# Kernel optimization log

Measured on AMD Instinct MI355X. Metric: run time of the kernel, lower is better.

## Reference

```python
import jax, jax.numpy as jnp
import numpy as np

E = 16      # num_experts
K = 4       # num_experts_per_tok
H = 2048    # hidden_size
I = 1408    # moe_intermediate_size
SI = 5632   # shared expert intermediate size
CAP = 1024
NORM_TOPK = False


def setup_inputs() -> dict:
    key = jax.random.key(0)
    ks = jax.random.split(key, 9)
    def w(k, shape, fan_in):
        return jax.random.normal(k, shape, jnp.float32) * (fan_in ** -0.5)
    return {
        "hidden_states": jax.random.normal(ks[0], (1, 2048, H), jnp.float32),
        "gate_w":  w(ks[1], (E, H), H),        # router: Linear(H -> E), no bias
        "we_gate": w(ks[2], (E, I, H), H),     # per-expert gate_proj weights
        "we_up":   w(ks[3], (E, I, H), H),     # per-expert up_proj weights
        "we_down": w(ks[4], (E, H, I), I),     # per-expert down_proj weights
        "ws_gate": w(ks[5], (SI, H), H),       # shared expert gate_proj
        "ws_up":   w(ks[6], (SI, H), H),       # shared expert up_proj
        "ws_down": w(ks[7], (H, SI), SI),      # shared expert down_proj
        "sg_w":    w(ks[8], (1, H), H),        # shared_expert_gate: Linear(H -> 1)
    }


def reference(hidden_states, gate_w, we_gate, we_up, we_down,
              ws_gate, ws_up, ws_down, sg_w):
    B, S, Hd = hidden_states.shape
    x = hidden_states.reshape(-1, Hd)                      # [T, H]
    T = x.shape[0]

    # --- router ---
    router_logits = x @ gate_w.T                           # [T, E]
    probs = jax.nn.softmax(router_logits.astype(jnp.float32), axis=-1)
    topw, topi = jax.lax.top_k(probs, K)                   # [T, K]
    if NORM_TOPK:
        topw = topw / topw.sum(axis=-1, keepdims=True)

    # --- dispatch: flatten (token, slot) assignments ---
    A = T * K
    fe = topi.reshape(A)                                   # expert id per assignment
    fw = topw.reshape(A)                                   # routing weight per assignment
    ft = jnp.repeat(jnp.arange(T), K)                      # token id per assignment
    # position of each assignment within its expert (rank in arrival order)
    oh = jax.nn.one_hot(fe, E, dtype=jnp.int32)            # [A, E]
    pos = jnp.take_along_axis(jnp.cumsum(oh, axis=0) - 1, fe[:, None], axis=1)[:, 0]
    valid = pos < CAP
    # scatter tokens into per-expert buffers; overflow goes to dummy row CAP
    buf = jnp.zeros((E, CAP + 1, Hd), x.dtype)
    buf = buf.at[fe, jnp.where(valid, pos, CAP)].set(x[ft])[:, :CAP]  # [E, C, H]

    # --- per-expert SiLU-gated MLP (batched grouped GEMMs) ---
    g = jnp.einsum('ech,eih->eci', buf, we_gate)
    u = jnp.einsum('ech,eih->eci', buf, we_up)
    eo = jnp.einsum('eci,ehi->ech', jax.nn.silu(g) * u, we_down)      # [E, C, H]

    # --- combine: weighted scatter-add back to tokens ---
    ga = eo[fe, jnp.minimum(pos, CAP - 1)]                 # [A, H]
    wcomb = (fw * valid.astype(fw.dtype)).astype(x.dtype)
    y = jnp.zeros((T, Hd), x.dtype).at[ft].add(ga * wcomb[:, None])

    # --- shared expert with sigmoid gate ---
    sh = (jax.nn.silu(x @ ws_gate.T) * (x @ ws_up.T)) @ ws_down.T
    sh = jax.nn.sigmoid(x @ sg_w.T) * sh

    out = (y + sh).reshape(B, S, Hd)
    return out, router_logits
```

## Files before the change

### kernel.cpp

```cpp
#include <hip/hip_runtime.h>

#define T_TOK 2048
#define NE 16
#define KTOP 4
#define HD 2048
#define ID 1408
#define SID 5632
#define CAPACITY 1024

typedef __attribute__((ext_vector_type(8))) short short8;
typedef __attribute__((ext_vector_type(4))) float floatx4;

__device__ __forceinline__ short f2b(float f){
  union { float f; unsigned u; } v; v.f = f;
  unsigned r = v.u + 0x7fffu + ((v.u >> 16) & 1u);
  return (short)(r >> 16);
}
__device__ __forceinline__ float b2f(short s){
  union { float f; unsigned u; } v; v.u = ((unsigned)(unsigned short)s) << 16;
  return v.f;
}
__device__ __forceinline__ unsigned cvt_pk(float a, float b){
  unsigned r;
  asm("v_cvt_pk_bf16_f32 %0, %1, %2" : "=v"(r) : "v"(a), "v"(b));
  return r;
}
__device__ __forceinline__ short8 cvt8(float4 a, float4 b){
  union { unsigned d[4]; short8 s; } u;
  u.d[0] = cvt_pk(a.x, a.y); u.d[1] = cvt_pk(a.z, a.w);
  u.d[2] = cvt_pk(b.x, b.y); u.d[3] = cvt_pk(b.z, b.w);
  return u.s;
}
__device__ __forceinline__ void gl16(const void* g, void* l){
  __builtin_amdgcn_global_load_lds(
      (const __attribute__((address_space(1))) void*)g,
      (__attribute__((address_space(3))) void*)l, 16, 0, 0);
}

__device__ __forceinline__ void conv_range(
    int cb, int ncb,
    const float* __restrict__ s1, short* __restrict__ d1, long long n1,
    const float* __restrict__ s2, short* __restrict__ d2, long long n2)
{
  const long long tot = n1 + n2;
  const long long stride = (long long)ncb * 256;
  #pragma unroll 2
  for (long long i = (long long)cb * 256 + threadIdx.x; i < tot; i += stride){
    const float* s; short8* d; long long j;
    if (i < n1){ s = s1; d = (short8*)d1; j = i; }
    else       { s = s2; d = (short8*)d2; j = i - n1; }
    float4 f0 = ((const float4*)s)[j * 2];
    float4 f1 = ((const float4*)s)[j * 2 + 1];
    d[j] = cvt8(f0, f1);
  }
}

__global__ void moe_zero(int* __restrict__ counts){
  if (threadIdx.x < NE) counts[threadIdx.x] = 0;
}

__global__ void moe_router(const float* __restrict__ x,
                           const float* __restrict__ gate_w,
                           const float* __restrict__ sg_w,
                           float* __restrict__ logits_out,
                           short* __restrict__ xb,
                           int* __restrict__ counts,
                           int* __restrict__ slot_token,
                           int* __restrict__ tslot,
                           float* __restrict__ tw,
                           float* __restrict__ sg,
                           const float* cs1, short* cd1, long long cn1,
                           const float* cs2, short* cd2, long long cn2)
{
  if (blockIdx.x >= 512){
    conv_range(blockIdx.x - 512, gridDim.x - 512, cs1, cd1, cn1, cs2, cd2, cn2);
    return;
  }
  int wave = threadIdx.x >> 6, lane = threadIdx.x & 63;
  int t = (blockIdx.x << 2) + wave;
  const float4* xr = (const float4*)(x + (size_t)t * HD);
  short8* xbw = (short8*)(xb + (size_t)t * HD);
  float acc[17];
  #pragma unroll
  for (int e = 0; e < 17; ++e) acc[e] = 0.f;
  #pragma unroll
  for (int j = 0; j < 4; ++j){
    int i4 = (j * 64 + lane) * 2;
    float4 x0 = xr[i4], x1 = xr[i4 + 1];
    xbw[j * 64 + lane] = cvt8(x0, x1);
    #pragma unroll
    for (int e = 0; e < 16; ++e){
      const float4* gr = (const float4*)(gate_w + e * HD);
      float4 g0 = gr[i4], g1 = gr[i4 + 1];
      acc[e] += x0.x*g0.x + x0.y*g0.y + x0.z*g0.z + x0.w*g0.w
              + x1.x*g1.x + x1.y*g1.y + x1.z*g1.z + x1.w*g1.w;
    }
    const float4* sr = (const float4*)sg_w;
    float4 s0 = sr[i4], s1 = sr[i4 + 1];
    acc[16] += x0.x*s0.x + x0.y*s0.y + x0.z*s0.z + x0.w*s0.w
             + x1.x*s1.x + x1.y*s1.y + x1.z*s1.z + x1.w*s1.w;
  }
  #pragma unroll
  for (int e = 0; e < 17; ++e){
    float v = acc[e];
    #pragma unroll
    for (int off = 32; off > 0; off >>= 1) v += __shfl_xor(v, off, 64);
    acc[e] = v;
  }
  if (lane == 0){
    float m = acc[0];
    #pragma unroll
    for (int e = 1; e < 16; ++e) m = fmaxf(m, acc[e]);
    float p[16]; float s = 0.f;
    #pragma unroll
    for (int e = 0; e < 16; ++e){ p[e] = expf(acc[e] - m); s += p[e]; }
    float inv = 1.f / s;
    #pragma unroll
    for (int e = 0; e < 16; ++e) logits_out[t * 16 + e] = acc[e];
    unsigned used = 0;
    for (int k = 0; k < KTOP; ++k){
      float best = -1.f; int bi = 0;
      #pragma unroll
      for (int e = 0; e < 16; ++e){
        float pe = ((used >> e) & 1u) ? -1.f : p[e];
        if (pe > best){ best = pe; bi = e; }
      }
      used |= (1u << bi);
      int pos = atomicAdd(&counts[bi], 1);
      int enc = -1;
      if (pos < CAPACITY){
        slot_token[bi * CAPACITY + pos] = t;
        enc = bi * CAPACITY + pos;
      }
      tslot[t * KTOP + k] = enc;
      tw[t * KTOP + k] = best * inv;
    }
    sg[t] = 1.f / (1.f + expf(-acc[16]));
  }
}


#define GEMM_PREAMBLE \
  const int tid = threadIdx.x; \
  const int lane = tid & 63, wave = tid >> 6; \
  const int wr = wave >> 1, wc = wave & 1; \
  const int lrow = lane & 15, lk = lane >> 4; \
  const int s_th = (tid & 7) ^ ((tid >> 3) & 7); \
  const int koff = (s_th & 3) << 3; \
  const int rloc = ((tid >> 3) << 1) + (s_th >> 2); \
  const int lb = lrow >> 1; \
  const int soff = (((((lrow & 1) << 2) | lk) ^ (lb & 7)) << 4); \
  const int abase = (wr * 32 + lb) * 128 + soff;

#define WAIT8  asm volatile("s_waitcnt vmcnt(8)" ::: "memory");
#define WAIT6  asm volatile("s_waitcnt vmcnt(6)" ::: "memory");
#define WAIT4  asm volatile("s_waitcnt vmcnt(4)" ::: "memory");
#define WAIT3  asm volatile("s_waitcnt vmcnt(3)" ::: "memory");
#define WAIT0  asm volatile("s_waitcnt vmcnt(0)" ::: "memory");
#define SBAR   asm volatile("s_barrier" ::: "memory");

__global__ __launch_bounds__(256) void moe_gateup(
    const short* __restrict__ Asrc,
    const short* __restrict__ Wg, const short* __restrict__ Wu,
    short* __restrict__ Out,
    const int* __restrict__ counts, const int* __restrict__ slot_token,
    int Ndim, int Kdim, int expert_mode, int mtiles, int ntiles,
    const float* cs1, short* cd1, long long cn1,
    const float* cs2, short* cd2, long long cn2, int conv_nwg)
{
  if ((int)blockIdx.x < conv_nwg){
    conv_range(blockIdx.x, conv_nwg, cs1, cd1, cn1, cs2, cd2, cn2);
    return;
  }
  int nwg = gridDim.x - conv_nwg;
  int bid = blockIdx.x - conv_nwg;
  int wg = ((bid & 7) * (nwg >> 3)) + (bid >> 3);
  int m_t = wg % mtiles; wg /= mtiles;
  int n_t = wg % ntiles; int e = wg / ntiles;

  int cnt = T_TOK; size_t woff = 0; short* out = Out;
  if (expert_mode){
    cnt = counts[e]; if (cnt > CAPACITY) cnt = CAPACITY;
    if (m_t * 128 >= cnt) return;
    woff = (size_t)e * Ndim * Kdim;
    out = Out + (size_t)e * CAPACITY * Ndim;
  }
  const int m0 = m_t * 128, n0 = n_t * 64;

  __shared__ __align__(16) char smem[3][16384];

  GEMM_PREAMBLE
  const int gbase = 8192 + (wc * 16 + lb) * 128 + soff;

  const short* aP0;
  const short* aP1;
  {
    int p0 = m0 + rloc, p1 = m0 + 64 + rloc;
    if (expert_mode){
      int q0 = (p0 < cnt) ? p0 : 0, q1 = (p1 < cnt) ? p1 : 0;
      aP0 = Asrc + (size_t)slot_token[e * CAPACITY + q0] * Kdim + koff;
      aP1 = Asrc + (size_t)slot_token[e * CAPACITY + q1] * Kdim + koff;
    } else {
      aP0 = Asrc + (size_t)p0 * Kdim + koff;
      aP1 = Asrc + (size_t)p1 * Kdim + koff;
    }
  }
  const short* bgP = Wg + woff + (size_t)(n0 + rloc) * Kdim + koff;
  const short* buP = Wu + woff + (size_t)(n0 + rloc) * Kdim + koff;

  const floatx4 vzero = {0.f, 0.f, 0.f, 0.f};
  floatx4 accg[4][2], accu[4][2];
  #pragma unroll
  for (int i = 0; i < 4; ++i)
    #pragma unroll
    for (int j = 0; j < 2; ++j){ accg[i][j] = vzero; accu[i][j] = vzero; }

#define GU_ISSUE(B, T) { char* _b = (B); const int _k = (T) << 5; \
    gl16(aP0 + _k, _b + tid * 16); \
    gl16(aP1 + _k, _b + 4096 + tid * 16); \
    gl16(bgP + _k, _b + 8192 + tid * 16); \
    gl16(buP + _k, _b + 12288 + tid * 16); }

#define GU_COMPUTE(B) { const char* bb = (B); \
    short8 a[4], bg[2], bu[2]; \
    _Pragma("unroll") \
    for (int mf = 0; mf < 4; ++mf) a[mf] = *(const short8*)(bb + abase + mf * 1024); \
    _Pragma("unroll") \
    for (int nf = 0; nf < 2; ++nf){ \
      bg[nf] = *(const short8*)(bb + gbase + nf * 1024); \
      bu[nf] = *(const short8*)(bb + gbase + 4096 + nf * 1024); } \
    _Pragma("unroll") \
    for (int mf = 0; mf < 4; ++mf) \
      _Pragma("unroll") \
      for (int nf = 0; nf < 2; ++nf){ \
        accg[mf][nf] = __builtin_amdgcn_mfma_f32_16x16x32_bf16(a[mf], bg[nf], accg[mf][nf], 0, 0, 0); \
        accu[mf][nf] = __builtin_amdgcn_mfma_f32_16x16x32_bf16(a[mf], bu[nf], accu[mf][nf], 0, 0, 0); } }

  const int NSTEP = Kdim >> 5;
  char* b0 = smem[0];
  char* b1 = smem[1];
  char* b2 = smem[2];
  GU_ISSUE(b0, 0)
  GU_ISSUE(b1, 1)
  for (int s = 0; s < NSTEP; ++s){
    if (s + 2 < NSTEP){ GU_ISSUE(b2, s + 2) WAIT8 }
    else if (s + 2 == NSTEP){ WAIT4 }
    else { WAIT0 }
    SBAR
    GU_COMPUTE(b0)
    SBAR
    char* t = b0; b0 = b1; b1 = b2; b2 = t;
  }

  const int colbase = n0 + wc * 32 + lrow;
  #pragma unroll
  for (int mf = 0; mf < 4; ++mf){
    int pr = m0 + wr * 64 + mf * 16 + lk * 4;
    #pragma unroll
    for (int nf = 0; nf < 2; ++nf){
      floatx4 g4 = accg[mf][nf], u4 = accu[mf][nf];
      int col = colbase + nf * 16;
      #pragma unroll
      for (int r = 0; r < 4; ++r){
        float gv = g4[r], uv = u4[r];
        float a = (gv / (1.f + __expf(-gv))) * uv;
        out[(size_t)(pr + r) * Ndim + col] = f2b(a);
      }
    }
  }
}

template<int NF>
__global__ __launch_bounds__(256) void moe_down(
    const short* __restrict__ Asrc, const short* __restrict__ Wd,
    float* __restrict__ y, short* __restrict__ eo,
    const int* __restrict__ counts, const int* __restrict__ slot_token,
    const float* __restrict__ sgate,
    int Kdim, int expert_mode, int mtiles, int ntiles)
{
  int nwg = gridDim.x;
  int wg = ((blockIdx.x & 7) * (nwg >> 3)) + (blockIdx.x >> 3);
  int m_t = wg % mtiles; wg /= mtiles;
  int n_t = wg % ntiles; int e = wg / ntiles;

  int cnt = T_TOK; const short* ab = Asrc; size_t woff = 0;
  if (expert_mode){
    cnt = counts[e]; if (cnt > CAPACITY) cnt = CAPACITY;
    if (m_t * 128 >= cnt) return;
    ab = Asrc + (size_t)e * CAPACITY * Kdim;
    woff = (size_t)e * HD * Kdim;
  }
  const int m0 = m_t * 128, n0 = n_t * (NF * 32);

  __shared__ __align__(16) char smem[3][8192 + NF * 2048];

  GEMM_PREAMBLE
  const int bbase = 8192 + (wc * (NF * 8) + lb) * 128 + soff;

  const short* aP0 = ab + (size_t)(m0 + rloc) * Kdim + koff;
  const short* aP1 = ab + (size_t)(m0 + 64 + rloc) * Kdim + koff;
  const short* bP0 = Wd + woff + (size_t)(n0 + rloc) * Kdim + koff;
  const short* bP1 = (NF == 4) ? (Wd + woff + (size_t)(n0 + 64 + rloc) * Kdim + koff) : bP0;

  const floatx4 vzero = {0.f, 0.f, 0.f, 0.f};
  floatx4 acc[4][NF];
  #pragma unroll
  for (int i = 0; i < 4; ++i)
    #pragma unroll
    for (int j = 0; j < NF; ++j) acc[i][j] = vzero;

#define DN_ISSUE(B, T) { char* _b = (B); const int _k = (T) << 5; \
    gl16(aP0 + _k, _b + tid * 16); \
    gl16(aP1 + _k, _b + 4096 + tid * 16); \
    gl16(bP0 + _k, _b + 8192 + tid * 16); \
    if (NF == 4) gl16(bP1 + _k, _b + 12288 + tid * 16); }

#define DN_COMPUTE(B) { const char* bb = (B); \
    short8 a[4], b[NF]; \
    _Pragma("unroll") \
    for (int mf = 0; mf < 4; ++mf) a[mf] = *(const short8*)(bb + abase + mf * 1024); \
    _Pragma("unroll") \
    for (int nf = 0; nf < NF; ++nf) b[nf] = *(const short8*)(bb + bbase + nf * 1024); \
    _Pragma("unroll") \
    for (int mf = 0; mf < 4; ++mf) \
      _Pragma("unroll") \
      for (int nf = 0; nf < NF; ++nf) \
        acc[mf][nf] = __builtin_amdgcn_mfma_f32_16x16x32_bf16(a[mf], b[nf], acc[mf][nf], 0, 0, 0); }

  const int NSTEP = Kdim >> 5;
  char* b0 = smem[0];
  char* b1 = smem[1];
  char* b2 = smem[2];
  DN_ISSUE(b0, 0)
  DN_ISSUE(b1, 1)
  for (int s = 0; s < NSTEP; ++s){
    if (s + 2 < NSTEP){
      DN_ISSUE(b2, s + 2)
      if (NF == 4){ WAIT8 } else { WAIT6 }
    } else if (s + 2 == NSTEP){
      if (NF == 4){ WAIT4 } else { WAIT3 }
    } else { WAIT0 }
    SBAR
    DN_COMPUTE(b0)
    SBAR
    char* t = b0; b0 = b1; b1 = b2; b2 = t;
  }

  const int colb = n0 + wc * (NF * 16) + lrow;
  if (expert_mode){
    #pragma unroll
    for (int mf = 0; mf < 4; ++mf){
      int pr = m0 + wr * 64 + mf * 16 + lk * 4;
      #pragma unroll
      for (int r = 0; r < 4; ++r){
        int p = pr + r;
        #pragma unroll
        for (int nf = 0; nf < NF; ++nf)
          eo[(size_t)(e * CAPACITY + p) * HD + colb + nf * 16] = f2b(acc[mf][nf][r]);
      }
    }
  } else {
    #pragma unroll
    for (int mf = 0; mf < 4; ++mf){
      int pr = m0 + wr * 64 + mf * 16 + lk * 4;
      #pragma unroll
      for (int r = 0; r < 4; ++r){
        int t = pr + r;
        float sv = sgate[t];
        #pragma unroll
        for (int nf = 0; nf < NF; ++nf)
          y[(size_t)t * HD + colb + nf * 16] = sv * acc[mf][nf][r];
      }
    }
  }
}

__global__ void moe_combine(const short* __restrict__ eo,
                            const int* __restrict__ tslot,
                            const float* __restrict__ tw,
                            float* __restrict__ y)
{
  int t = blockIdx.x;
  int o = threadIdx.x << 3;
  float* yp = y + (size_t)t * HD + o;
  float4 a0 = *(const float4*)yp, a1 = *(const float4*)(yp + 4);
  float acc[8] = {a0.x, a0.y, a0.z, a0.w, a1.x, a1.y, a1.z, a1.w};
  #pragma unroll
  for (int k = 0; k < KTOP; ++k){
    int s = tslot[t * KTOP + k];
    if (s >= 0){
      float w = tw[t * KTOP + k];
      short8 v = *(const short8*)(eo + (size_t)s * HD + o);
      #pragma unroll
      for (int j = 0; j < 8; ++j) acc[j] += w * b2f(v[j]);
    }
  }
  float4 r0 = {acc[0], acc[1], acc[2], acc[3]};
  float4 r1 = {acc[4], acc[5], acc[6], acc[7]};
  *(float4*)yp = r0; *(float4*)(yp + 4) = r1;
}

extern "C" void kernel_launch(void* const* d_in, const int* in_sizes, int n_in,
                              void* d_out, int out_size, void* d_ws, size_t ws_size,
                              hipStream_t stream)
{
  (void)in_sizes; (void)n_in; (void)out_size; (void)ws_size;
  const float* x       = (const float*)d_in[0];
  const float* gate_w  = (const float*)d_in[1];
  const float* we_gate = (const float*)d_in[2];
  const float* we_up   = (const float*)d_in[3];
  const float* we_down = (const float*)d_in[4];
  const float* wsg     = (const float*)d_in[5];
  const float* wsu     = (const float*)d_in[6];
  const float* wsd     = (const float*)d_in[7];
  const float* sg_w    = (const float*)d_in[8];

  float* y      = (float*)d_out;
  float* logits = y + (size_t)T_TOK * HD;

  const size_t N_EW = (size_t)NE * ID * HD;
  const size_t N_SW = (size_t)SID * HD;
  const long long G_EW = (long long)(N_EW / 8);
  const long long G_SW = (long long)(N_SW / 8);

  char* ws = (char*)d_ws;
  size_t off = 0;
  short* xb   = (short*)(ws + off); off += (size_t)T_TOK * HD * 2;
  short* wb   = (short*)(ws + off); off += (3 * N_EW + 3 * N_SW) * 2;
  short* act  = (short*)(ws + off); off += (size_t)NE * CAPACITY * ID * 2;
  short* acts = (short*)(ws + off); off += (size_t)T_TOK * SID * 2;
  int*   slot_token = (int*)  (ws + off); off += 65536;
  int*   tslot      = (int*)  (ws + off); off += 32768;
  float* tw         = (float*)(ws + off); off += 32768;
  int*   counts     = (int*)  (ws + off); off += 256;
  float* sg         = (float*)(ws + off);

  short* wbeg = wb;
  short* wbeu = wb + N_EW;
  short* wbed = wb + 2 * N_EW;
  short* wbsg = wb + 3 * N_EW;
  short* wbsu = wb + 3 * N_EW + N_SW;
  short* wbsd = wb + 3 * N_EW + 2 * N_SW;
  short* eo = wbeg;

  moe_zero<<<1, 64, 0, stream>>>(counts);
  moe_router<<<512 + 512, 256, 0, stream>>>(x, gate_w, sg_w, logits, xb,
                                            counts, slot_token, tslot, tw, sg,
                                            wsg, wbsg, G_SW, wsu, wbsu, G_SW);
  moe_gateup<<<512 + 16 * 88, 256, 0, stream>>>(xb, wbsg, wbsu, acts,
                                                nullptr, nullptr, SID, HD, 0, 16, 88,
                                                we_gate, wbeg, G_EW, we_up, wbeu, G_EW, 512);
  moe_gateup<<<512 + 8 * 22 * NE, 256, 0, stream>>>(xb, wbeg, wbeu, act,
                                                    counts, slot_token, ID, HD, 1, 8, 22,
                                                    we_down, wbed, G_EW, wsd, wbsd, G_SW, 512);
  moe_down<2><<<16 * 32, 256, 0, stream>>>(acts, wbsd, y, nullptr, nullptr, nullptr,
                                           sg, SID, 0, 16, 32);
  moe_down<4><<<8 * 16 * NE, 256, 0, stream>>>(act, wbed, y, eo, counts, slot_token,
                                               nullptr, ID, 1, 8, 16);
  moe_combine<<<T_TOK, 256, 0, stream>>>(eo, tslot, tw, y);
}
```

Before: 759.6 us.

## Load fp32 weights directly into GEMMs and convert to bf16 in-register

Removes the separate fp32-to-bf16 weight conversion passes that were folded into the router and gate/up launches. The GEMM kernels now stream fp32 weight tiles into LDS and convert them to bf16 while building MFMA operands. This drops the full write and re-read of bf16 weight copies, at the cost of twice the weight bytes per tile in the GEMM loops. The LDS pipeline also goes from triple to double buffering to fit the larger fp32 tiles, which reduces load/compute overlap.

After: 918.4 us. +20.9%, slower.

```diff
diff --git a/kernel.cpp b/kernel.cpp
--- a/kernel.cpp
+++ b/kernel.cpp
@@ -35,24 +35,6 @@
   __builtin_amdgcn_global_load_lds(
       (const __attribute__((address_space(1))) void*)g,
       (__attribute__((address_space(3))) void*)l, 16, 0, 0);
-}
-
-__device__ __forceinline__ void conv_range(
-    int cb, int ncb,
-    const float* __restrict__ s1, short* __restrict__ d1, long long n1,
-    const float* __restrict__ s2, short* __restrict__ d2, long long n2)
-{
-  const long long tot = n1 + n2;
-  const long long stride = (long long)ncb * 256;
-  #pragma unroll 2
-  for (long long i = (long long)cb * 256 + threadIdx.x; i < tot; i += stride){
-    const float* s; short8* d; long long j;
-    if (i < n1){ s = s1; d = (short8*)d1; j = i; }
-    else       { s = s2; d = (short8*)d2; j = i - n1; }
-    float4 f0 = ((const float4*)s)[j * 2];
-    float4 f1 = ((const float4*)s)[j * 2 + 1];
-    d[j] = cvt8(f0, f1);
-  }
 }
 
 __global__ void moe_zero(int* __restrict__ counts){
@@ -68,14 +50,8 @@
                            int* __restrict__ slot_token,
                            int* __restrict__ tslot,
                            float* __restrict__ tw,
-                           float* __restrict__ sg,
-                           const float* cs1, short* cd1, long long cn1,
-                           const float* cs2, short* cd2, long long cn2)
+                           float* __restrict__ sg)
 {
-  if (blockIdx.x >= 512){
-    conv_range(blockIdx.x - 512, gridDim.x - 512, cs1, cd1, cn1, cs2, cd2, cn2);
-    return;
-  }
   int wave = threadIdx.x >> 6, lane = threadIdx.x & 63;
   int t = (blockIdx.x << 2) + wave;
   const float4* xr = (const float4*)(x + (size_t)t * HD);
@@ -150,31 +126,26 @@
   const int rloc = ((tid >> 3) << 1) + (s_th >> 2); \
   const int lb = lrow >> 1; \
   const int soff = (((((lrow & 1) << 2) | lk) ^ (lb & 7)) << 4); \
-  const int abase = (wr * 32 + lb) * 128 + soff;
-
-#define WAIT8  asm volatile("s_waitcnt vmcnt(8)" ::: "memory");
+  const int abase = (wr * 32 + lb) * 128 + soff; \
+  const int srow8 = tid >> 3; \
+  const int bls = (tid & 7) ^ (srow8 & 7); \
+  const int xr_ = lrow & 7; \
+  const int sl0 = ((lk << 1) ^ xr_) << 4, sl1 = (((lk << 1) | 1) ^ xr_) << 4;
+
 #define WAIT6  asm volatile("s_waitcnt vmcnt(6)" ::: "memory");
 #define WAIT4  asm volatile("s_waitcnt vmcnt(4)" ::: "memory");
-#define WAIT3  asm volatile("s_waitcnt vmcnt(3)" ::: "memory");
 #define WAIT0  asm volatile("s_waitcnt vmcnt(0)" ::: "memory");
 #define SBAR   asm volatile("s_barrier" ::: "memory");
 
 __global__ __launch_bounds__(256) void moe_gateup(
     const short* __restrict__ Asrc,
-    const short* __restrict__ Wg, const short* __restrict__ Wu,
+    const float* __restrict__ Wg, const float* __restrict__ Wu,
     short* __restrict__ Out,
     const int* __restrict__ counts, const int* __restrict__ slot_token,
-    int Ndim, int Kdim, int expert_mode, int mtiles, int ntiles,
-    const float* cs1, short* cd1, long long cn1,
-    const float* cs2, short* cd2, long long cn2, int conv_nwg)
+    int Ndim, int Kdim, int expert_mode, int mtiles, int ntiles)
 {
-  if ((int)blockIdx.x < conv_nwg){
-    conv_range(blockIdx.x, conv_nwg, cs1, cd1, cn1, cs2, cd2, cn2);
-    return;
-  }
-  int nwg = gridDim.x - conv_nwg;
-  int bid = blockIdx.x - conv_nwg;
-  int wg = ((bid & 7) * (nwg >> 3)) + (bid >> 3);
+  int nwg = gridDim.x;
+  int wg = ((blockIdx.x & 7) * (nwg >> 3)) + (blockIdx.x >> 3);
   int m_t = wg % mtiles; wg /= mtiles;
   int n_t = wg % ntiles; int e = wg / ntiles;
 
@@ -187,10 +158,9 @@
   }
   const int m0 = m_t * 128, n0 = n_t * 64;
 
-  __shared__ __align__(16) char smem[3][16384];
+  __shared__ __align__(16) char smem[2][24576];
 
   GEMM_PREAMBLE
-  const int gbase = 8192 + (wc * 16 + lb) * 128 + soff;
 
   const short* aP0;
   const short* aP1;
@@ -205,8 +175,14 @@
       aP1 = Asrc + (size_t)p1 * Kdim + koff;
     }
   }
-  const short* bgP = Wg + woff + (size_t)(n0 + rloc) * Kdim + koff;
-  const short* buP = Wu + woff + (size_t)(n0 + rloc) * Kdim + koff;
+  const float* bgP0 = Wg + woff + (size_t)(n0 + srow8) * Kdim + bls * 4;
+  const float* bgP1 = Wg + woff + (size_t)(n0 + 32 + srow8) * Kdim + bls * 4;
+  const float* buP0 = Wu + woff + (size_t)(n0 + srow8) * Kdim + bls * 4;
+  const float* buP1 = Wu + woff + (size_t)(n0 + 32 + srow8) * Kdim + bls * 4;
+
+  const int rg0 = wc * 32 + lrow, rg1 = rg0 + 16;
+  const int o00 = rg0 * 128 + sl0, o01 = rg0 * 128 + sl1;
+  const int o10 = rg1 * 128 + sl0, o11 = rg1 * 128 + sl1;
 
   const floatx4 vzero = {0.f, 0.f, 0.f, 0.f};
   floatx4 accg[4][2], accu[4][2];
@@ -218,17 +194,19 @@
 #define GU_ISSUE(B, T) { char* _b = (B); const int _k = (T) << 5; \
     gl16(aP0 + _k, _b + tid * 16); \
     gl16(aP1 + _k, _b + 4096 + tid * 16); \
-    gl16(bgP + _k, _b + 8192 + tid * 16); \
-    gl16(buP + _k, _b + 12288 + tid * 16); }
+    gl16(bgP0 + _k, _b + 8192 + tid * 16); \
+    gl16(bgP1 + _k, _b + 12288 + tid * 16); \
+    gl16(buP0 + _k, _b + 16384 + tid * 16); \
+    gl16(buP1 + _k, _b + 20480 + tid * 16); }
 
 #define GU_COMPUTE(B) { const char* bb = (B); \
     short8 a[4], bg[2], bu[2]; \
     _Pragma("unroll") \
     for (int mf = 0; mf < 4; ++mf) a[mf] = *(const short8*)(bb + abase + mf * 1024); \
-    _Pragma("unroll") \
-    for (int nf = 0; nf < 2; ++nf){ \
-      bg[nf] = *(const short8*)(bb + gbase + nf * 1024); \
-      bu[nf] = *(const short8*)(bb + gbase + 4096 + nf * 1024); } \
+    bg[0] = cvt8(*(const float4*)(bb + 8192 + o00), *(const float4*)(bb + 8192 + o01)); \
+    bg[1] = cvt8(*(const float4*)(bb + 8192 + o10), *(const float4*)(bb + 8192 + o11)); \
+    bu[0] = cvt8(*(const float4*)(bb + 16384 + o00), *(const float4*)(bb + 16384 + o01)); \
+    bu[1] = cvt8(*(const float4*)(bb + 16384 + o10), *(const float4*)(bb + 16384 + o11)); \
     _Pragma("unroll") \
     for (int mf = 0; mf < 4; ++mf) \
       _Pragma("unroll") \
@@ -237,19 +215,13 @@
         accu[mf][nf] = __builtin_amdgcn_mfma_f32_16x16x32_bf16(a[mf], bu[nf], accu[mf][nf], 0, 0, 0); } }
 
   const int NSTEP = Kdim >> 5;
-  char* b0 = smem[0];
-  char* b1 = smem[1];
-  char* b2 = smem[2];
-  GU_ISSUE(b0, 0)
-  GU_ISSUE(b1, 1)
+  GU_ISSUE(smem[0], 0)
   for (int s = 0; s < NSTEP; ++s){
-    if (s + 2 < NSTEP){ GU_ISSUE(b2, s + 2) WAIT8 }
-    else if (s + 2 == NSTEP){ WAIT4 }
+    if (s + 1 < NSTEP){ GU_ISSUE(smem[(s + 1) & 1], s + 1) WAIT6 }
     else { WAIT0 }
     SBAR
-    GU_COMPUTE(b0)
+    GU_COMPUTE(smem[s & 1])
     SBAR
-    char* t = b0; b0 = b1; b1 = b2; b2 = t;
   }
 
   const int colbase = n0 + wc * 32 + lrow;
@@ -272,7 +244,7 @@
 
 template<int NF>
 __global__ __launch_bounds__(256) void moe_down(
-    const short* __restrict__ Asrc, const short* __restrict__ Wd,
+    const short* __restrict__ Asrc, const float* __restrict__ Wd,
     float* __restrict__ y, short* __restrict__ eo,
     const int* __restrict__ counts, const int* __restrict__ slot_token,
     const float* __restrict__ sgate,
@@ -292,15 +264,23 @@
   }
   const int m0 = m_t * 128, n0 = n_t * (NF * 32);
 
-  __shared__ __align__(16) char smem[3][8192 + NF * 2048];
+  __shared__ __align__(16) char smem[2][8192 + NF * 4096];
 
   GEMM_PREAMBLE
-  const int bbase = 8192 + (wc * (NF * 8) + lb) * 128 + soff;
 
   const short* aP0 = ab + (size_t)(m0 + rloc) * Kdim + koff;
   const short* aP1 = ab + (size_t)(m0 + 64 + rloc) * Kdim + koff;
-  const short* bP0 = Wd + woff + (size_t)(n0 + rloc) * Kdim + koff;
-  const short* bP1 = (NF == 4) ? (Wd + woff + (size_t)(n0 + 64 + rloc) * Kdim + koff) : bP0;
+  const float* bP[NF];
+  #pragma unroll
+  for (int i = 0; i < NF; ++i)
+    bP[i] = Wd + woff + (size_t)(n0 + i * 32 + srow8) * Kdim + bls * 4;
+
+  int bo0[NF], bo1[NF];
+  #pragma unroll
+  for (int nf = 0; nf < NF; ++nf){
+    int r = wc * (NF * 16) + nf * 16 + lrow;
+    bo0[nf] = r * 128 + sl0; bo1[nf] = r * 128 + sl1;
+  }
 
   const floatx4 vzero = {0.f, 0.f, 0.f, 0.f};
   floatx4 acc[4][NF];
@@ -312,15 +292,18 @@
 #define DN_ISSUE(B, T) { char* _b = (B); const int _k = (T) << 5; \
     gl16(aP0 + _k, _b + tid * 16); \
     gl16(aP1 + _k, _b + 4096 + tid * 16); \
-    gl16(bP0 + _k, _b + 8192 + tid * 16); \
-    if (NF == 4) gl16(bP1 + _k, _b + 12288 + tid * 16); }
+    _Pragma("unroll") \
+    for (int i = 0; i < NF; ++i) \
+      gl16(bP[i] + _k, _b + 8192 + i * 4096 + tid * 16); }
 
 #define DN_COMPUTE(B) { const char* bb = (B); \
     short8 a[4], b[NF]; \
     _Pragma("unroll") \
     for (int mf = 0; mf < 4; ++mf) a[mf] = *(const short8*)(bb + abase + mf * 1024); \
     _Pragma("unroll") \
-    for (int nf = 0; nf < NF; ++nf) b[nf] = *(const short8*)(bb + bbase + nf * 1024); \
+    for (int nf = 0; nf < NF; ++nf) \
+      b[nf] = cvt8(*(const float4*)(bb + 8192 + bo0[nf]), \
+                   *(const float4*)(bb + 8192 + bo1[nf])); \
     _Pragma("unroll") \
     for (int mf = 0; mf < 4; ++mf) \
       _Pragma("unroll") \
@@ -328,22 +311,15 @@
         acc[mf][nf] = __builtin_amdgcn_mfma_f32_16x16x32_bf16(a[mf], b[nf], acc[mf][nf], 0, 0, 0); }
 
   const int NSTEP = Kdim >> 5;
-  char* b0 = smem[0];
-  char* b1 = smem[1];
-  char* b2 = smem[2];
-  DN_ISSUE(b0, 0)
-  DN_ISSUE(b1, 1)
+  DN_ISSUE(smem[0], 0)
   for (int s = 0; s < NSTEP; ++s){
-    if (s + 2 < NSTEP){
-      DN_ISSUE(b2, s + 2)
-      if (NF == 4){ WAIT8 } else { WAIT6 }
-    } else if (s + 2 == NSTEP){
-      if (NF == 4){ WAIT4 } else { WAIT3 }
+    if (s + 1 < NSTEP){
+      DN_ISSUE(smem[(s + 1) & 1], s + 1)
+      if (NF == 4){ WAIT6 } else { WAIT4 }
     } else { WAIT0 }
     SBAR
-    DN_COMPUTE(b0)
+    DN_COMPUTE(smem[s & 1])
     SBAR
-    char* t = b0; b0 = b1; b1 = b2; b2 = t;
   }
 
   const int colb = n0 + wc * (NF * 16) + lrow;
@@ -418,44 +394,28 @@
   float* y      = (float*)d_out;
   float* logits = y + (size_t)T_TOK * HD;
 
-  const size_t N_EW = (size_t)NE * ID * HD;
-  const size_t N_SW = (size_t)SID * HD;
-  const long long G_EW = (long long)(N_EW / 8);
-  const long long G_SW = (long long)(N_SW / 8);
-
   char* ws = (char*)d_ws;
   size_t off = 0;
   short* xb   = (short*)(ws + off); off += (size_t)T_TOK * HD * 2;
-  short* wb   = (short*)(ws + off); off += (3 * N_EW + 3 * N_SW) * 2;
   short* act  = (short*)(ws + off); off += (size_t)NE * CAPACITY * ID * 2;
   short* acts = (short*)(ws + off); off += (size_t)T_TOK * SID * 2;
+  short* eo   = (short*)(ws + off); off += (size_t)NE * CAPACITY * HD * 2;
   int*   slot_token = (int*)  (ws + off); off += 65536;
   int*   tslot      = (int*)  (ws + off); off += 32768;
   float* tw         = (float*)(ws + off); off += 32768;
   int*   counts     = (int*)  (ws + off); off += 256;
   float* sg         = (float*)(ws + off);
 
-  short* wbeg = wb;
-  short* wbeu = wb + N_EW;
-  short* wbed = wb + 2 * N_EW;
-  short* wbsg = wb + 3 * N_EW;
-  short* wbsu = wb + 3 * N_EW + N_SW;
-  short* wbsd = wb + 3 * N_EW + 2 * N_SW;
-  short* eo = wbeg;
-
   moe_zero<<<1, 64, 0, stream>>>(counts);
-  moe_router<<<512 + 512, 256, 0, stream>>>(x, gate_w, sg_w, logits, xb,
-                                            counts, slot_token, tslot, tw, sg,
-                                            wsg, wbsg, G_SW, wsu, wbsu, G_SW);
-  moe_gateup<<<512 + 16 * 88, 256, 0, stream>>>(xb, wbsg, wbsu, acts,
-                                                nullptr, nullptr, SID, HD, 0, 16, 88,
-                                                we_gate, wbeg, G_EW, we_up, wbeu, G_EW, 512);
-  moe_gateup<<<512 + 8 * 22 * NE, 256, 0, stream>>>(xb, wbeg, wbeu, act,
-                                                    counts, slot_token, ID, HD, 1, 8, 22,
-                                                    we_down, wbed, G_EW, wsd, wbsd, G_SW, 512);
-  moe_down<2><<<16 * 32, 256, 0, stream>>>(acts, wbsd, y, nullptr, nullptr, nullptr,
+  moe_router<<<512, 256, 0, stream>>>(x, gate_w, sg_w, logits, xb,
+                                      counts, slot_token, tslot, tw, sg);
+  moe_gateup<<<16 * 88, 256, 0, stream>>>(xb, wsg, wsu, acts,
+                                          nullptr, nullptr, SID, HD, 0, 16, 88);
+  moe_gateup<<<8 * 22 * NE, 256, 0, stream>>>(xb, we_gate, we_up, act,
+                                              counts, slot_token, ID, HD, 1, 8, 22);
+  moe_down<2><<<16 * 32, 256, 0, stream>>>(acts, wsd, y, nullptr, nullptr, nullptr,
                                            sg, SID, 0, 16, 32);
-  moe_down<4><<<8 * 16 * NE, 256, 0, stream>>>(act, wbed, y, eo, counts, slot_token,
+  moe_down<4><<<8 * 16 * NE, 256, 0, stream>>>(act, we_down, y, eo, counts, slot_token,
                                                nullptr, ID, 1, 8, 16);
   moe_combine<<<T_TOK, 256, 0, stream>>>(eo, tslot, tw, y);
 }
```
